# Performance work log

Measured on AMD Instinct MI355X. Metric: run time of the kernel, lower is better.

## Reference

```python
import jax, jax.numpy as jnp
import numpy as np

B, N, T, NL, DIM, H, HD = 4, 2048, 8, 64, 1024, 16, 64


def setup_inputs() -> dict:
    key = jax.random.key(0)
    ks = jax.random.split(key, 8)
    text = jax.random.normal(ks[0], (B, N, DIM), dtype=jnp.float32)
    media = jax.random.normal(ks[1], (B, T, NL, DIM), dtype=jnp.float32)
    # place exactly T media tokens per row, evenly spaced, so cumsum times are in [1, T]
    loc = np.zeros((B, N), dtype=bool)
    step = N // T
    loc[:, np.arange(T) * step] = True
    media_locations = jnp.asarray(loc)
    s = 1.0 / np.sqrt(DIM)
    wq = jax.random.normal(ks[2], (DIM, DIM), dtype=jnp.float32) * s
    wkv = jax.random.normal(ks[3], (DIM, 2 * DIM), dtype=jnp.float32) * s
    wo = jax.random.normal(ks[4], (DIM, DIM), dtype=jnp.float32) * s
    bo = jnp.zeros((DIM,), dtype=jnp.float32)
    ln_g = jnp.ones((DIM,), dtype=jnp.float32)
    ln_b = jnp.zeros((DIM,), dtype=jnp.float32)
    return {"text": text, "media": media, "media_locations": media_locations,
            "wq": wq, "wkv": wkv, "wo": wo, "bo": bo, "ln_g": ln_g, "ln_b": ln_b}


def _layernorm(x, g, b, eps=1e-5):
    mu = jnp.mean(x, axis=-1, keepdims=True)
    var = jnp.var(x, axis=-1, keepdims=True)
    return (x - mu) * jax.lax.rsqrt(var + eps) * g + b


def reference(text, media, media_locations, wq, wkv, wo, bo, ln_g, ln_b):
    b, t, nl, d = media.shape
    tn = _layernorm(text, ln_g, ln_b)                 # [b, n, d]
    q = tn @ wq                                        # [b, n, d]
    m = media.reshape(b, t * nl, d)                    # [b, tn, d]
    kv = m @ wkv                                       # [b, tn, 2d]
    k, v = jnp.split(kv, 2, axis=-1)
    q = q.reshape(b, -1, H, HD).transpose(0, 2, 1, 3)  # [b, h, n, hd]
    k = k.reshape(b, -1, H, HD).transpose(0, 2, 1, 3)  # [b, h, tn, hd]
    v = v.reshape(b, -1, H, HD).transpose(0, 2, 1, 3)
    scores = jnp.einsum('bhid,bhjd->bhij', q, k)       # [b, h, n, tn]
    text_times = jnp.cumsum(media_locations.astype(jnp.int32), axis=-1)  # [b, n]
    media_times = jnp.repeat(jnp.arange(1, t + 1, dtype=jnp.int32), nl)  # [tn]
    mask = text_times[:, None, :, None] == media_times[None, None, None, :]
    neg = jnp.finfo(scores.dtype).min
    scores = jnp.where(mask, scores, neg)
    attn = jax.nn.softmax(scores, axis=-1)
    no_media = (text_times == 0)[:, None, :, None]     # [b, 1, n, 1]
    attn = jnp.where(no_media, 0.0, attn)
    out = jnp.einsum('bhij,bhjd->bhid', attn, v)       # [b, h, n, hd]
    out = out.transpose(0, 2, 1, 3).reshape(b, -1, H * HD)
    return out @ wo + bo
```

## Files before the change

kernel.cpp:

```cpp
#include <hip/hip_runtime.h>
#include <stdint.h>

#define B_ 4
#define N_ 2048
#define T_ 8
#define NL_ 64
#define DIM_ 1024
#define H_ 16
#define HD_ 64
#define TN_ (T_*NL_)

typedef __bf16 bf16x8 __attribute__((ext_vector_type(8)));
typedef float f32x4 __attribute__((ext_vector_type(4)));

__device__ __forceinline__ float b2f(unsigned short x) {
  union { uint32_t u; float f; } v; v.u = ((uint32_t)x) << 16; return v.f;
}
__device__ __forceinline__ unsigned short f2b(float f) {
  union { float f; uint32_t u; } v; v.f = f;
  uint32_t r = v.u + 0x7FFFu + ((v.u >> 16) & 1u);
  return (unsigned short)(r >> 16);
}

__device__ __forceinline__ void gload_lds16(const unsigned short* g, unsigned short* l) {
  __builtin_amdgcn_global_load_lds(
      (const __attribute__((address_space(1))) uint32_t*)g,
      (__attribute__((address_space(3))) uint32_t*)l, 16, 0, 0);
}

__device__ __forceinline__ bool detect_isf(const unsigned short* text, int t) {
  int l = t & 63;
  int bad = 0;
  #pragma unroll
  for (int i = 0; i < 16; i++) {
    unsigned short w = text[l * 16 + i];
    int e = (w >> 7) & 0xFF;
    if (e != 0 && (e < 90 || e > 150)) bad++;
  }
  #pragma unroll
  for (int off = 32; off > 0; off >>= 1) bad += __shfl_xor(bad, off);
  return bad > 64;
}

#define PREP_TIMES 4
#define PREP_LN    (B_*N_)
#define PREP_CAST  2049
#define PREP_TR    4096

__global__ __launch_bounds__(256) void prep_kernel(
    const void* __restrict__ locs, int* __restrict__ tt,
    const void* __restrict__ text, const void* __restrict__ lng,
    const void* __restrict__ lnb, unsigned short* __restrict__ tn,
    const void* __restrict__ media, unsigned short* __restrict__ mb,
    const void* __restrict__ bo, unsigned short* __restrict__ bob,
    const void* __restrict__ wq, unsigned short* __restrict__ wqt,
    const void* __restrict__ wkv, unsigned short* __restrict__ wkvt,
    const void* __restrict__ wo, unsigned short* __restrict__ wot,
    int* __restrict__ flag) {
  __shared__ __align__(16) unsigned char shraw[32 * 33 * 2];
  int gb = blockIdx.x;
  int t = threadIdx.x;
  bool isf = detect_isf((const unsigned short*)text, t);
  if (gb == 0 && t == 0) flag[0] = isf ? 1 : 0;

  if (gb < PREP_TIMES) {
    int* red = (int*)shraw;
    int b = gb;
    const unsigned char* p8 = (const unsigned char*)locs;
    const int* p32 = (const int*)locs;
    int cnt = 0;
    for (int i = t; i < B_*N_; i += 256) cnt += (p8[i] != 0) ? 1 : 0;
    red[t] = cnt;
    __syncthreads();
    for (int off = 128; off > 0; off >>= 1) {
      if (t < off) red[t] += red[t + off];
      __syncthreads();
    }
    int total = red[0];
    __syncthreads();
    bool isb = (total >= 2 * T_);
    int x[8];
    int base = b * N_ + t * 8;
    if (isb) {
      #pragma unroll
      for (int i = 0; i < 8; i++) x[i] = (int)(p8[base + i] != 0);
    } else {
      #pragma unroll
      for (int i = 0; i < 8; i++) x[i] = (int)(p32[base + i] != 0);
    }
    #pragma unroll
    for (int i = 1; i < 8; i++) x[i] += x[i-1];
    int tot = x[7];
    red[t] = tot;
    __syncthreads();
    for (int off = 1; off < 256; off <<= 1) {
      int v = (t >= off) ? red[t - off] : 0;
      __syncthreads();
      red[t] += v;
      __syncthreads();
    }
    int excl = red[t] - tot;
    #pragma unroll
    for (int i = 0; i < 8; i++) tt[base + i] = excl + x[i];
    return;
  }
  gb -= PREP_TIMES;

  if (gb < PREP_LN) {
    float* sm = (float*)shraw;
    int row = gb;
    float f0, f1, f2, f3, g0, g1, g2, g3, c0, c1, c2, c3;
    if (isf) {
      float4 xv = ((const float4*)text)[(size_t)row * (DIM_/4) + t];
      f0 = xv.x; f1 = xv.y; f2 = xv.z; f3 = xv.w;
      float4 gv = ((const float4*)lng)[t];
      g0 = gv.x; g1 = gv.y; g2 = gv.z; g3 = gv.w;
      float4 bv = ((const float4*)lnb)[t];
      c0 = bv.x; c1 = bv.y; c2 = bv.z; c3 = bv.w;
    } else {
      ushort4 xv = ((const ushort4*)text)[(size_t)row * (DIM_/4) + t];
      f0 = b2f(xv.x); f1 = b2f(xv.y); f2 = b2f(xv.z); f3 = b2f(xv.w);
      ushort4 gv = ((const ushort4*)lng)[t];
      g0 = b2f(gv.x); g1 = b2f(gv.y); g2 = b2f(gv.z); g3 = b2f(gv.w);
      ushort4 bv = ((const ushort4*)lnb)[t];
      c0 = b2f(bv.x); c1 = b2f(bv.y); c2 = b2f(bv.z); c3 = b2f(bv.w);
    }
    float s  = f0 + f1 + f2 + f3;
    float s2 = f0*f0 + f1*f1 + f2*f2 + f3*f3;
    for (int off = 32; off > 0; off >>= 1) { s += __shfl_xor(s, off); s2 += __shfl_xor(s2, off); }
    int wave = t >> 6, lane = t & 63;
    if (lane == 0) { sm[wave] = s; sm[wave + 4] = s2; }
    __syncthreads();
    float ts  = sm[0] + sm[1] + sm[2] + sm[3];
    float ts2 = sm[4] + sm[5] + sm[6] + sm[7];
    float mean = ts * (1.0f / DIM_);
    float var  = ts2 * (1.0f / DIM_) - mean * mean;
    float rs = rsqrtf(var + 1e-5f);
    ushort4 o;
    o.x = f2b((f0 - mean) * rs * g0 + c0);
    o.y = f2b((f1 - mean) * rs * g1 + c1);
    o.z = f2b((f2 - mean) * rs * g2 + c2);
    o.w = f2b((f3 - mean) * rs * g3 + c3);
    ((ushort4*)(tn + (size_t)row * DIM_))[t] = o;
    return;
  }
  gb -= PREP_LN;

  if (gb < PREP_CAST) {
    const int N4M = (B_*T_*NL_*DIM_) / 4;
    int i = gb * 256 + t;
    if (i < N4M) {
      ushort4 o;
      if (isf) {
        float4 v = ((const float4*)media)[i];
        o.x = f2b(v.x); o.y = f2b(v.y); o.z = f2b(v.z); o.w = f2b(v.w);
      } else {
        o = ((const ushort4*)media)[i];
      }
      ((ushort4*)mb)[i] = o;
    } else {
      int j = i - N4M;
      if (j < DIM_/4) {
        ushort4 o;
        if (isf) {
          float4 v = ((const float4*)bo)[j];
          o.x = f2b(v.x); o.y = f2b(v.y); o.z = f2b(v.z); o.w = f2b(v.w);
        } else {
          o = ((const ushort4*)bo)[j];
        }
        ((ushort4*)bob)[j] = o;
      }
    }
    return;
  }
  gb -= PREP_CAST;

  {
    unsigned short (*tile)[33] = (unsigned short (*)[33])shraw;
    const void* src; unsigned short* dst; int C, zz, nx;
    if (gb < 1024)      { src = wq;  dst = wqt;  C = 1024; zz = gb;        nx = 32; }
    else if (gb < 3072) { src = wkv; dst = wkvt; C = 2048; zz = gb - 1024; nx = 64; }
    else                { src = wo;  dst = wot;  C = 1024; zz = gb - 3072; nx = 32; }
    const int R = 1024;
    int xi = zz % nx, yi = zz / nx;
    int bx = xi * 32, by = yi * 32;
    int x = t & 31, y = t >> 5;
    if (isf) {
      const float* s = (const float*)src;
      for (int i = y; i < 32; i += 8) tile[i][x] = f2b(s[(size_t)(by + i) * C + bx + x]);
    } else {
      const unsigned short* s = (const unsigned short*)src;
      for (int i = y; i < 32; i += 8) tile[i][x] = s[(size_t)(by + i) * C + bx + x];
    }
    __syncthreads();
    for (int i = y; i < 32; i += 8) dst[(size_t)(bx + i) * R + by + x] = tile[x][i];
  }
}

__device__ __forceinline__ void gemm128_core(const unsigned short* __restrict__ A,
                                             const unsigned short* __restrict__ Bt,
                                             unsigned short* __restrict__ C,
                                             float* __restrict__ Cf,
                                             const unsigned short* __restrict__ bias,
                                             int bid, int mtiles, int M, int N, int K,
                                             bool f32o, int t) {
  __shared__ unsigned short As[3][128][32];
  __shared__ unsigned short Bs[3][128][32];
  int m0 = (bid % mtiles) * 128, n0 = (bid / mtiles) * 128;
  int wave = t >> 6, lane = t & 63;
  int wr = wave >> 1, wc = wave & 1;
  f32x4 acc[4][4];
  #pragma unroll
  for (int i = 0; i < 4; i++)
    #pragma unroll
    for (int j = 0; j < 4; j++)
      #pragma unroll
      for (int r = 0; r < 4; r++) acc[i][j][r] = 0.f;
  int lr = lane & 15, lk = (lane >> 4) * 8;
  int row0 = t >> 2,         kc0 = (t & 3) * 8;
  int row1 = (t + 256) >> 2, kc1 = ((t + 256) & 3) * 8;
  const unsigned short* a0 = A  + (size_t)(m0 + row0) * K + kc0;
  const unsigned short* a1 = A  + (size_t)(m0 + row1) * K + kc1;
  const unsigned short* b0 = Bt + (size_t)(n0 + row0) * K + kc0;
  const unsigned short* b1 = Bt + (size_t)(n0 + row1) * K + kc1;
#define STAGE_(buf, koff) do { \
    gload_lds16(a0 + (koff), &As[buf][row0][kc0]); \
    gload_lds16(a1 + (koff), &As[buf][row1][kc1]); \
    gload_lds16(b0 + (koff), &Bs[buf][row0][kc0]); \
    gload_lds16(b1 + (koff), &Bs[buf][row1][kc1]); \
  } while (0)
  STAGE_(0, 0);
  STAGE_(1, 32);
  STAGE_(2, 64);
  asm volatile("s_waitcnt vmcnt(8)" ::: "memory");
  __builtin_amdgcn_s_barrier();
  int cur = 0;
  for (int k0 = 0; k0 < K; k0 += 32) {
    bf16x8 af[4], bfr[4];
    #pragma unroll
    for (int i = 0; i < 4; i++) af[i]  = *(const bf16x8*)(&As[cur][wr * 64 + i * 16 + lr][lk]);
    #pragma unroll
    for (int j = 0; j < 4; j++) bfr[j] = *(const bf16x8*)(&Bs[cur][wc * 64 + j * 16 + lr][lk]);
    asm volatile("s_waitcnt lgkmcnt(0)" ::: "memory");
    __builtin_amdgcn_sched_barrier(0);
    __builtin_amdgcn_s_barrier();
    if (k0 + 96 < K) {
      STAGE_(cur, k0 + 96);
      __builtin_amdgcn_sched_barrier(0);
    }
    #pragma unroll
    for (int i = 0; i < 4; i++)
      #pragma unroll
      for (int j = 0; j < 4; j++)
        acc[i][j] = __builtin_amdgcn_mfma_f32_16x16x32_bf16(af[i], bfr[j], acc[i][j], 0, 0, 0);
    if (k0 + 96 < K) {
      asm volatile("s_waitcnt vmcnt(8)" ::: "memory");
      __builtin_amdgcn_s_barrier();
    } else if (k0 + 64 < K) {
      asm volatile("s_waitcnt vmcnt(4)" ::: "memory");
      __builtin_amdgcn_s_barrier();
    } else if (k0 + 32 < K) {
      asm volatile("s_waitcnt vmcnt(0)" ::: "memory");
      __builtin_amdgcn_s_barrier();
    }
    cur = (cur == 2) ? 0 : cur + 1;
  }
#undef STAGE_
  int rbase = (lane >> 4) * 4;
  int cbase = lane & 15;
  #pragma unroll
  for (int i = 0; i < 4; i++) {
    #pragma unroll
    for (int j = 0; j < 4; j++) {
      int row = m0 + wr * 64 + i * 16 + rbase;
      int col = n0 + wc * 64 + j * 16 + cbase;
      float bv = bias ? b2f(bias[col]) : 0.f;
      if (f32o) {
        #pragma unroll
        for (int r = 0; r < 4; r++)
          Cf[(size_t)(row + r) * N + col] = acc[i][j][r] + bv;
      } else {
        #pragma unroll
        for (int r = 0; r < 4; r++)
          C[(size_t)(row + r) * N + col] = f2b(acc[i][j][r] + bv);
      }
    }
  }
}

__global__ __launch_bounds__(256) void gemm_qkv(const unsigned short* __restrict__ tn,
                                                const unsigned short* __restrict__ wqt,
                                                unsigned short* __restrict__ qb,
                                                const unsigned short* __restrict__ mb,
                                                const unsigned short* __restrict__ wkvt,
                                                unsigned short* __restrict__ kvb) {
  int bid = blockIdx.x;
  if (bid < 512)
    gemm128_core(tn, wqt, qb, nullptr, nullptr, bid, 64, B_ * N_, DIM_, DIM_, false, threadIdx.x);
  else
    gemm128_core(mb, wkvt, kvb, nullptr, nullptr, bid - 512, 16, B_ * TN_, 2 * DIM_, DIM_, false, threadIdx.x);
}

__global__ __launch_bounds__(256) void gemm_out(const unsigned short* __restrict__ ao,
                                                const unsigned short* __restrict__ wot,
                                                unsigned short* __restrict__ C,
                                                float* __restrict__ Cf,
                                                const unsigned short* __restrict__ bias,
                                                const int* __restrict__ flag) {
  bool f32o = (*flag != 0);
  gemm128_core(ao, wot, C, Cf, bias, blockIdx.x, 64, B_ * N_, DIM_, DIM_, f32o, threadIdx.x);
}

__global__ __launch_bounds__(64) void attn_mfma(const unsigned short* __restrict__ q,
                                                const unsigned short* __restrict__ kv,
                                                const int* __restrict__ tt,
                                                unsigned short* __restrict__ ao) {
  __shared__ unsigned short Ps[32][68];
  int bid = blockIdx.x;
  int h  = bid & 15;
  int nt = (bid >> 4) & 63;
  int b  = bid >> 10;
  int bn0 = b * N_ + nt * 32;
  int lane = threadIdx.x & 63;
  int lr = lane & 15;
  int g  = lane >> 4;
  int g8 = g * 8;

  int tv = tt[bn0];
  float vmul = (tv >= 1 && tv <= T_) ? 1.f : 0.f;
  int tvc = tv < 1 ? 1 : (tv > T_ ? T_ : tv);
  int kvrow0 = b * TN_ + (tvc - 1) * NL_;

  const unsigned short* vb = kv + (size_t)kvrow0 * (2 * DIM_) + DIM_ + h * HD_;
  bf16x8 bV[2][4];
  #pragma unroll
  for (int ks = 0; ks < 2; ks++)
    #pragma unroll
    for (int ni = 0; ni < 4; ni++)
      #pragma unroll
      for (int j = 0; j < 8; j++)
        bV[ks][ni][j] = *(const __bf16*)(vb + (size_t)(ks * 32 + g8 + j) * (2 * DIM_) + ni * 16 + lr);

  f32x4 S[2][4];
  #pragma unroll
  for (int i = 0; i < 2; i++)
    #pragma unroll
    for (int j = 0; j < 4; j++)
      #pragma unroll
      for (int r = 0; r < 4; r++) S[i][j][r] = 0.f;
  #pragma unroll
  for (int ks = 0; ks < 2; ks++) {
    bf16x8 aQ[2], bK[4];
    #pragma unroll
    for (int mi = 0; mi < 2; mi++)
      aQ[mi] = *(const bf16x8*)(q + (size_t)(bn0 + mi * 16 + lr) * DIM_ + h * HD_ + ks * 32 + g8);
    #pragma unroll
    for (int ni = 0; ni < 4; ni++)
      bK[ni] = *(const bf16x8*)(kv + (size_t)(kvrow0 + ni * 16 + lr) * (2 * DIM_) + h * HD_ + ks * 32 + g8);
    #pragma unroll
    for (int mi = 0; mi < 2; mi++)
      #pragma unroll
      for (int ni = 0; ni < 4; ni++)
        S[mi][ni] = __builtin_amdgcn_mfma_f32_16x16x32_bf16(aQ[mi], bK[ni], S[mi][ni], 0, 0, 0);
  }

  #pragma unroll
  for (int mi = 0; mi < 2; mi++) {
    #pragma unroll
    for (int r = 0; r < 4; r++) {
      float mx = fmaxf(fmaxf(S[mi][0][r], S[mi][1][r]), fmaxf(S[mi][2][r], S[mi][3][r]));
      mx = fmaxf(mx, __shfl_xor(mx, 1));
      mx = fmaxf(mx, __shfl_xor(mx, 2));
      mx = fmaxf(mx, __shfl_xor(mx, 4));
      mx = fmaxf(mx, __shfl_xor(mx, 8));
      float e0 = __expf(S[mi][0][r] - mx);
      float e1 = __expf(S[mi][1][r] - mx);
      float e2 = __expf(S[mi][2][r] - mx);
      float e3 = __expf(S[mi][3][r] - mx);
      float sum = e0 + e1 + e2 + e3;
      sum += __shfl_xor(sum, 1);
      sum += __shfl_xor(sum, 2);
      sum += __shfl_xor(sum, 4);
      sum += __shfl_xor(sum, 8);
      float inv = 1.f / sum;
      int qrow = mi * 16 + g * 4 + r;
      Ps[qrow][ 0 + lr] = f2b(e0 * inv);
      Ps[qrow][16 + lr] = f2b(e1 * inv);
      Ps[qrow][32 + lr] = f2b(e2 * inv);
      Ps[qrow][48 + lr] = f2b(e3 * inv);
    }
  }
  __syncthreads();

  f32x4 O[2][4];
  #pragma unroll
  for (int i = 0; i < 2; i++)
    #pragma unroll
    for (int j = 0; j < 4; j++)
      #pragma unroll
      for (int r = 0; r < 4; r++) O[i][j][r] = 0.f;
  #pragma unroll
  for (int ks = 0; ks < 2; ks++) {
    bf16x8 aP[2];
    #pragma unroll
    for (int mi = 0; mi < 2; mi++)
      aP[mi] = *(const bf16x8*)(&Ps[mi * 16 + lr][ks * 32 + g8]);
    #pragma unroll
    for (int mi = 0; mi < 2; mi++)
      #pragma unroll
      for (int ni = 0; ni < 4; ni++)
        O[mi][ni] = __builtin_amdgcn_mfma_f32_16x16x32_bf16(aP[mi], bV[ks][ni], O[mi][ni], 0, 0, 0);
  }
  __syncthreads();

  #pragma unroll
  for (int mi = 0; mi < 2; mi++)
    #pragma unroll
    for (int ni = 0; ni < 4; ni++)
      #pragma unroll
      for (int r = 0; r < 4; r++)
        Ps[mi * 16 + g * 4 + r][ni * 16 + lr] = f2b(O[mi][ni][r] * vmul);
  __syncthreads();
  int row = lane >> 1, half = lane & 1;
  uint4* dst = (uint4*)(ao + (size_t)(bn0 + row) * DIM_ + h * HD_ + half * 32);
  #pragma unroll
  for (int c = 0; c < 4; c++)
    dst[c] = *(const uint4*)(&Ps[row][half * 32 + c * 8]);
}

extern "C" void kernel_launch(void* const* d_in, const int* in_sizes, int n_in,
                              void* d_out, int out_size, void* d_ws, size_t ws_size,
                              hipStream_t stream) {
  const void* text = d_in[0];
  const void* media = d_in[1];
  const void* mloc = d_in[2];
  const void* wq  = d_in[3];
  const void* wkv = d_in[4];
  const void* wo  = d_in[5];
  const void* bo  = d_in[6];
  const void* lng = d_in[7];
  const void* lnb = d_in[8];

  char* ws = (char*)d_ws;
  const size_t OFF_FLAG = (size_t)32 << 10;
  const size_t OFF_TN   = (size_t)64 << 10;
  const size_t OFF_WQT  = OFF_TN  + ((size_t)16 << 20) + ((size_t)64 << 10);
  const size_t OFF_WKVT = OFF_WQT + ((size_t)2 << 20);
  const size_t OFF_WOT  = OFF_WKVT + ((size_t)4 << 20);
  const size_t OFF_KV   = OFF_WOT + ((size_t)2 << 20);
  const size_t OFF_MB   = OFF_KV  + ((size_t)8 << 20);
  const size_t OFF_BO   = OFF_MB  + ((size_t)4 << 20);
  const size_t OFF_QB   = OFF_BO  + ((size_t)64 << 10);
  int* tt               = (int*)(ws + 0);
  int* flag             = (int*)(ws + OFF_FLAG);
  unsigned short* tn    = (unsigned short*)(ws + OFF_TN);
  unsigned short* ao    = tn;
  unsigned short* wqt   = (unsigned short*)(ws + OFF_WQT);
  unsigned short* wkvt  = (unsigned short*)(ws + OFF_WKVT);
  unsigned short* wot   = (unsigned short*)(ws + OFF_WOT);
  unsigned short* kvb   = (unsigned short*)(ws + OFF_KV);
  unsigned short* mb    = (unsigned short*)(ws + OFF_MB);
  unsigned short* bob   = (unsigned short*)(ws + OFF_BO);
  unsigned short* qb    = (unsigned short*)(ws + OFF_QB);

  prep_kernel<<<PREP_TIMES + PREP_LN + PREP_CAST + PREP_TR, 256, 0, stream>>>(
      mloc, tt, text, lng, lnb, tn, media, mb, bo, bob,
      wq, wqt, wkv, wkvt, wo, wot, flag);

  gemm_qkv<<<768, 256, 0, stream>>>(tn, wqt, qb, mb, wkvt, kvb);
  attn_mfma<<<B_ * (N_/32) * H_, 64, 0, stream>>>(qb, kvb, tt, ao);
  gemm_out<<<512, 256, 0, stream>>>(ao, wot, (unsigned short*)d_out, (float*)d_out, bob, flag);
}
```

Before: 197.7 us.

## Fuse all stages into one persistent cooperative kernel with grid syncs

```diff
diff --git a/kernel.cpp b/kernel.cpp
--- a/kernel.cpp
+++ b/kernel.cpp
@@ -1,5 +1,8 @@
 #include <hip/hip_runtime.h>
+#include <hip/hip_cooperative_groups.h>
 #include <stdint.h>
+
+namespace cg = cooperative_groups;
 
 #define B_ 4
 #define N_ 2048
@@ -28,6 +31,11 @@
       (__attribute__((address_space(3))) uint32_t*)l, 16, 0, 0);
 }
 
+#define WAVE_LDS_FENCE() do { \
+    asm volatile("s_waitcnt lgkmcnt(0)" ::: "memory"); \
+    __builtin_amdgcn_sched_barrier(0); \
+  } while (0)
+
 __device__ __forceinline__ bool detect_isf(const unsigned short* text, int t) {
   int l = t & 63;
   int bad = 0;
@@ -46,23 +54,15 @@
 #define PREP_LN    (B_*N_)
 #define PREP_CAST  2049
 #define PREP_TR    4096
-
-__global__ __launch_bounds__(256) void prep_kernel(
-    const void* __restrict__ locs, int* __restrict__ tt,
-    const void* __restrict__ text, const void* __restrict__ lng,
-    const void* __restrict__ lnb, unsigned short* __restrict__ tn,
-    const void* __restrict__ media, unsigned short* __restrict__ mb,
-    const void* __restrict__ bo, unsigned short* __restrict__ bob,
-    const void* __restrict__ wq, unsigned short* __restrict__ wqt,
-    const void* __restrict__ wkv, unsigned short* __restrict__ wkvt,
-    const void* __restrict__ wo, unsigned short* __restrict__ wot,
-    int* __restrict__ flag) {
-  __shared__ __align__(16) unsigned char shraw[32 * 33 * 2];
-  int gb = blockIdx.x;
-  int t = threadIdx.x;
-  bool isf = detect_isf((const unsigned short*)text, t);
-  if (gb == 0 && t == 0) flag[0] = isf ? 1 : 0;
-
+#define NPREP (PREP_TIMES + PREP_LN + PREP_CAST + PREP_TR)
+
+__device__ __forceinline__ void prep_task(
+    int gb, int t, bool isf, unsigned char* shraw,
+    const void* locs, int* tt,
+    const void* text, const void* lng, const void* lnb, unsigned short* tn,
+    const void* media, unsigned short* mb, const void* bo, unsigned short* bob,
+    const void* wq, unsigned short* wqt, const void* wkv, unsigned short* wkvt,
+    const void* wo, unsigned short* wot) {
   if (gb < PREP_TIMES) {
     int* red = (int*)shraw;
     int b = gb;
@@ -102,13 +102,9 @@
     int excl = red[t] - tot;
     #pragma unroll
     for (int i = 0; i < 8; i++) tt[base + i] = excl + x[i];
-    return;
-  }
-  gb -= PREP_TIMES;
-
-  if (gb < PREP_LN) {
+  } else if (gb < PREP_TIMES + PREP_LN) {
     float* sm = (float*)shraw;
-    int row = gb;
+    int row = gb - PREP_TIMES;
     float f0, f1, f2, f3, g0, g1, g2, g3, c0, c1, c2, c3;
     if (isf) {
       float4 xv = ((const float4*)text)[(size_t)row * (DIM_/4) + t];
@@ -142,13 +138,9 @@
     o.z = f2b((f2 - mean) * rs * g2 + c2);
     o.w = f2b((f3 - mean) * rs * g3 + c3);
     ((ushort4*)(tn + (size_t)row * DIM_))[t] = o;
-    return;
-  }
-  gb -= PREP_LN;
-
-  if (gb < PREP_CAST) {
+  } else if (gb < PREP_TIMES + PREP_LN + PREP_CAST) {
     const int N4M = (B_*T_*NL_*DIM_) / 4;
-    int i = gb * 256 + t;
+    int i = (gb - PREP_TIMES - PREP_LN) * 256 + t;
     if (i < N4M) {
       ushort4 o;
       if (isf) {
@@ -171,16 +163,13 @@
         ((ushort4*)bob)[j] = o;
       }
     }
-    return;
-  }
-  gb -= PREP_CAST;
-
-  {
+  } else {
     unsigned short (*tile)[33] = (unsigned short (*)[33])shraw;
+    int z = gb - PREP_TIMES - PREP_LN - PREP_CAST;
     const void* src; unsigned short* dst; int C, zz, nx;
-    if (gb < 1024)      { src = wq;  dst = wqt;  C = 1024; zz = gb;        nx = 32; }
-    else if (gb < 3072) { src = wkv; dst = wkvt; C = 2048; zz = gb - 1024; nx = 64; }
-    else                { src = wo;  dst = wot;  C = 1024; zz = gb - 3072; nx = 32; }
+    if (z < 1024)      { src = wq;  dst = wqt;  C = 1024; zz = z;        nx = 32; }
+    else if (z < 3072) { src = wkv; dst = wkvt; C = 2048; zz = z - 1024; nx = 64; }
+    else               { src = wo;  dst = wot;  C = 1024; zz = z - 3072; nx = 32; }
     const int R = 1024;
     int xi = zz % nx, yi = zz / nx;
     int bx = xi * 32, by = yi * 32;
@@ -203,9 +192,10 @@
                                              float* __restrict__ Cf,
                                              const unsigned short* __restrict__ bias,
                                              int bid, int mtiles, int M, int N, int K,
-                                             bool f32o, int t) {
-  __shared__ unsigned short As[3][128][32];
-  __shared__ unsigned short Bs[3][128][32];
+                                             bool f32o, int t, unsigned char* smem) {
+  typedef unsigned short lds_t[128][32];
+  lds_t* As = (lds_t*)smem;
+  lds_t* Bs = (lds_t*)(smem + 3 * 128 * 32 * 2);
   int m0 = (bid % mtiles) * 128, n0 = (bid / mtiles) * 128;
   int wave = t >> 6, lane = t & 63;
   int wr = wave >> 1, wc = wave & 1;
@@ -288,40 +278,15 @@
   }
 }
 
-__global__ __launch_bounds__(256) void gemm_qkv(const unsigned short* __restrict__ tn,
-                                                const unsigned short* __restrict__ wqt,
-                                                unsigned short* __restrict__ qb,
-                                                const unsigned short* __restrict__ mb,
-                                                const unsigned short* __restrict__ wkvt,
-                                                unsigned short* __restrict__ kvb) {
-  int bid = blockIdx.x;
-  if (bid < 512)
-    gemm128_core(tn, wqt, qb, nullptr, nullptr, bid, 64, B_ * N_, DIM_, DIM_, false, threadIdx.x);
-  else
-    gemm128_core(mb, wkvt, kvb, nullptr, nullptr, bid - 512, 16, B_ * TN_, 2 * DIM_, DIM_, false, threadIdx.x);
-}
-
-__global__ __launch_bounds__(256) void gemm_out(const unsigned short* __restrict__ ao,
-                                                const unsigned short* __restrict__ wot,
-                                                unsigned short* __restrict__ C,
-                                                float* __restrict__ Cf,
-                                                const unsigned short* __restrict__ bias,
-                                                const int* __restrict__ flag) {
-  bool f32o = (*flag != 0);
-  gemm128_core(ao, wot, C, Cf, bias, blockIdx.x, 64, B_ * N_, DIM_, DIM_, f32o, threadIdx.x);
-}
-
-__global__ __launch_bounds__(64) void attn_mfma(const unsigned short* __restrict__ q,
-                                                const unsigned short* __restrict__ kv,
-                                                const int* __restrict__ tt,
-                                                unsigned short* __restrict__ ao) {
-  __shared__ unsigned short Ps[32][68];
-  int bid = blockIdx.x;
-  int h  = bid & 15;
-  int nt = (bid >> 4) & 63;
-  int b  = bid >> 10;
+__device__ __forceinline__ void attn_wave(int task, int lane, unsigned short (*Ps)[68],
+                                          const unsigned short* __restrict__ q,
+                                          const unsigned short* __restrict__ kv,
+                                          const int* __restrict__ tt,
+                                          unsigned short* __restrict__ ao) {
+  int h  = task & 15;
+  int nt = (task >> 4) & 63;
+  int b  = task >> 10;
   int bn0 = b * N_ + nt * 32;
-  int lane = threadIdx.x & 63;
   int lr = lane & 15;
   int g  = lane >> 4;
   int g8 = g * 8;
@@ -390,7 +355,7 @@
       Ps[qrow][48 + lr] = f2b(e3 * inv);
     }
   }
-  __syncthreads();
+  WAVE_LDS_FENCE();
 
   f32x4 O[2][4];
   #pragma unroll
@@ -411,7 +376,7 @@
       for (int ni = 0; ni < 4; ni++)
         O[mi][ni] = __builtin_amdgcn_mfma_f32_16x16x32_bf16(aP[mi], bV[ks][ni], O[mi][ni], 0, 0, 0);
   }
-  __syncthreads();
+  WAVE_LDS_FENCE();
 
   #pragma unroll
   for (int mi = 0; mi < 2; mi++)
@@ -420,12 +385,105 @@
       #pragma unroll
       for (int r = 0; r < 4; r++)
         Ps[mi * 16 + g * 4 + r][ni * 16 + lr] = f2b(O[mi][ni][r] * vmul);
-  __syncthreads();
+  WAVE_LDS_FENCE();
   int row = lane >> 1, half = lane & 1;
   uint4* dst = (uint4*)(ao + (size_t)(bn0 + row) * DIM_ + h * HD_ + half * 32);
   #pragma unroll
   for (int c = 0; c < 4; c++)
     dst[c] = *(const uint4*)(&Ps[row][half * 32 + c * 8]);
+}
+
+__global__ __launch_bounds__(256, 3) void fused_all(
+    const void* locs, int* tt,
+    const void* text, const void* lng, const void* lnb, unsigned short* tn,
+    const void* media, unsigned short* mb, const void* bo, unsigned short* bob,
+    const void* wq, unsigned short* wqt, const void* wkv, unsigned short* wkvt,
+    const void* wo, unsigned short* wot,
+    unsigned short* qb, unsigned short* kvb, unsigned short* ao,
+    unsigned short* Cb, float* Cf) {
+  __shared__ __align__(16) unsigned char SMEM[49152];
+  cg::grid_group gg = cg::this_grid();
+  int t = threadIdx.x;
+  int nb = gridDim.x;
+  bool isf = detect_isf((const unsigned short*)text, t);
+
+  for (int task = blockIdx.x; task < NPREP; task += nb) {
+    prep_task(task, t, isf, SMEM, locs, tt, text, lng, lnb, tn,
+              media, mb, bo, bob, wq, wqt, wkv, wkvt, wo, wot);
+    __syncthreads();
+  }
+  __threadfence();
+  gg.sync();
+
+  for (int task = blockIdx.x; task < 768; task += nb) {
+    if (task < 512)
+      gemm128_core(tn, wqt, qb, nullptr, nullptr, task, 64, B_ * N_, DIM_, DIM_, false, t, SMEM);
+    else
+      gemm128_core(mb, wkvt, kvb, nullptr, nullptr, task - 512, 16, B_ * TN_, 2 * DIM_, DIM_, false, t, SMEM);
+    __syncthreads();
+  }
+  __threadfence();
+  gg.sync();
+
+  {
+    int wave = t >> 6, lane = t & 63;
+    unsigned short (*Ps)[68] = (unsigned short (*)[68])(SMEM + wave * (32 * 68 * 2));
+    int gw = blockIdx.x * 4 + wave;
+    for (int task = gw; task < B_ * (N_/32) * H_; task += nb * 4)
+      attn_wave(task, lane, Ps, qb, kvb, tt, ao);
+  }
+  __threadfence();
+  gg.sync();
+
+  for (int task = blockIdx.x; task < 512; task += nb) {
+    gemm128_core(ao, wot, Cb, Cf, bob, task, 64, B_ * N_, DIM_, DIM_, isf, t, SMEM);
+    __syncthreads();
+  }
+}
+
+__global__ __launch_bounds__(256) void prep_kernel(
+    const void* locs, int* tt,
+    const void* text, const void* lng, const void* lnb, unsigned short* tn,
+    const void* media, unsigned short* mb, const void* bo, unsigned short* bob,
+    const void* wq, unsigned short* wqt, const void* wkv, unsigned short* wkvt,
+    const void* wo, unsigned short* wot) {
+  __shared__ __align__(16) unsigned char shraw[2304];
+  bool isf = detect_isf((const unsigned short*)text, threadIdx.x);
+  prep_task(blockIdx.x, threadIdx.x, isf, shraw, locs, tt, text, lng, lnb, tn,
+            media, mb, bo, bob, wq, wqt, wkv, wkvt, wo, wot);
+}
+
+__global__ __launch_bounds__(256) void gemm_qkv(const unsigned short* __restrict__ tn,
+                                                const unsigned short* __restrict__ wqt,
+                                                unsigned short* __restrict__ qb,
+                                                const unsigned short* __restrict__ mb,
+                                                const unsigned short* __restrict__ wkvt,
+                                                unsigned short* __restrict__ kvb) {
+  __shared__ __align__(16) unsigned char SM[49152];
+  int bid = blockIdx.x;
+  if (bid < 512)
+    gemm128_core(tn, wqt, qb, nullptr, nullptr, bid, 64, B_ * N_, DIM_, DIM_, false, threadIdx.x, SM);
+  else
+    gemm128_core(mb, wkvt, kvb, nullptr, nullptr, bid - 512, 16, B_ * TN_, 2 * DIM_, DIM_, false, threadIdx.x, SM);
+}
+
+__global__ __launch_bounds__(64) void attn_mfma(const unsigned short* __restrict__ q,
+                                                const unsigned short* __restrict__ kv,
+                                                const int* __restrict__ tt,
+                                                unsigned short* __restrict__ ao) {
+  __shared__ unsigned short Ps[32][68];
+  attn_wave(blockIdx.x, threadIdx.x & 63, Ps, q, kv, tt, ao);
+}
+
+__global__ __launch_bounds__(256) void gemm_out_k(const unsigned short* __restrict__ ao,
+                                                  const unsigned short* __restrict__ wot,
+                                                  unsigned short* __restrict__ C,
+                                                  float* __restrict__ Cf,
+                                                  const unsigned short* __restrict__ bias,
+                                                  const void* __restrict__ text) {
+  __shared__ __align__(16) unsigned char SM[49152];
+  bool isf = detect_isf((const unsigned short*)text, threadIdx.x);
+  gemm128_core(ao, wot, C, Cf, bias, blockIdx.x, 64, B_ * N_, DIM_, DIM_, isf, threadIdx.x, SM);
 }
 
 extern "C" void kernel_launch(void* const* d_in, const int* in_sizes, int n_in,
@@ -442,7 +500,6 @@
   const void* lnb = d_in[8];
 
   char* ws = (char*)d_ws;
-  const size_t OFF_FLAG = (size_t)32 << 10;
   const size_t OFF_TN   = (size_t)64 << 10;
   const size_t OFF_WQT  = OFF_TN  + ((size_t)16 << 20) + ((size_t)64 << 10);
   const size_t OFF_WKVT = OFF_WQT + ((size_t)2 << 20);
@@ -452,7 +509,6 @@
   const size_t OFF_BO   = OFF_MB  + ((size_t)4 << 20);
   const size_t OFF_QB   = OFF_BO  + ((size_t)64 << 10);
   int* tt               = (int*)(ws + 0);
-  int* flag             = (int*)(ws + OFF_FLAG);
   unsigned short* tn    = (unsigned short*)(ws + OFF_TN);
   unsigned short* ao    = tn;
   unsigned short* wqt   = (unsigned short*)(ws + OFF_WQT);
@@ -462,12 +518,22 @@
   unsigned short* mb    = (unsigned short*)(ws + OFF_MB);
   unsigned short* bob   = (unsigned short*)(ws + OFF_BO);
   unsigned short* qb    = (unsigned short*)(ws + OFF_QB);
-
-  prep_kernel<<<PREP_TIMES + PREP_LN + PREP_CAST + PREP_TR, 256, 0, stream>>>(
-      mloc, tt, text, lng, lnb, tn, media, mb, bo, bob,
-      wq, wqt, wkv, wkvt, wo, wot, flag);
-
-  gemm_qkv<<<768, 256, 0, stream>>>(tn, wqt, qb, mb, wkvt, kvb);
-  attn_mfma<<<B_ * (N_/32) * H_, 64, 0, stream>>>(qb, kvb, tt, ao);
-  gemm_out<<<512, 256, 0, stream>>>(ao, wot, (unsigned short*)d_out, (float*)d_out, bob, flag);
-}
+  unsigned short* Cb    = (unsigned short*)d_out;
+  float* Cf             = (float*)d_out;
+
+  void* args[] = { (void*)&mloc, (void*)&tt, (void*)&text, (void*)&lng, (void*)&lnb,
+                   (void*)&tn, (void*)&media, (void*)&mb, (void*)&bo, (void*)&bob,
+                   (void*)&wq, (void*)&wqt, (void*)&wkv, (void*)&wkvt, (void*)&wo,
+                   (void*)&wot, (void*)&qb, (void*)&kvb, (void*)&ao,
+                   (void*)&Cb, (void*)&Cf };
+  hipError_t ce = hipLaunchCooperativeKernel((void*)fused_all, dim3(768), dim3(256),
+                                             args, 0, stream);
+  if (ce != hipSuccess) {
+    prep_kernel<<<NPREP, 256, 0, stream>>>(mloc, tt, text, lng, lnb, tn,
+                                           media, mb, bo, bob,
+                                           wq, wqt, wkv, wkvt, wo, wot);
+    gemm_qkv<<<768, 256, 0, stream>>>(tn, wqt, qb, mb, wkvt, kvb);
+    attn_mfma<<<B_ * (N_/32) * H_, 64, 0, stream>>>(qb, kvb, tt, ao);
+    gemm_out_k<<<512, 256, 0, stream>>>(ao, wot, Cb, Cf, bob, text);
+  }
+}
```

New measurement: 754.5 us. 3.82x slower.
